# Kernel optimization log

Hardware: AMD Instinct MI355X
Metric: run time of the kernel (lower is better)

The kernel has to match this reference:

```python
import jax, jax.numpy as jnp
import numpy as np

H = 16        # num_heads
D = 128       # head_dim = hidden_size // num_heads
HID = 2048    # hidden_size
BLOCK = 64    # moba_chunk_size
TOPK = 8      # moba_topk


def setup_inputs() -> dict:
    key = jax.random.key(0)
    ks = jax.random.split(key, 5)
    B, S = 1, 2048
    hidden_states = jax.random.normal(ks[0], (B, S, HID), dtype=jnp.float32)
    scale = HID ** -0.5
    Wq = jax.random.normal(ks[1], (HID, H * D), dtype=jnp.float32) * scale
    Wk = jax.random.normal(ks[2], (HID, H * D), dtype=jnp.float32) * scale
    Wv = jax.random.normal(ks[3], (HID, H * D), dtype=jnp.float32) * scale
    Wo = jax.random.normal(ks[4], (H * D, HID), dtype=jnp.float32) * scale
    return {"hidden_states": hidden_states, "Wq": Wq, "Wk": Wk, "Wv": Wv, "Wo": Wo}


def _moba_forward(hidden_states, Wq, Wk, Wv, Wo):
    B, S, _ = hidden_states.shape
    nb = S // BLOCK
    INF = jnp.float32(jnp.inf)

    q = (hidden_states @ Wq).reshape(B, S, H, D)
    k = (hidden_states @ Wk).reshape(B, S, H, D)
    v = (hidden_states @ Wv).reshape(B, S, H, D)

    # MoBA gating: mean-pooled key per block -> [B, nb, H, D]
    kg = k.reshape(B, nb, BLOCK, H, D).mean(axis=2)
    gate = jnp.einsum('bshd,bnhd->bhsn', q, kg)  # [B,H,S,nb]

    pos = jnp.arange(S)
    qb = pos // BLOCK                 # query's own block
    blk = jnp.arange(nb)
    is_self = qb[:, None] == blk[None, :]                      # self block always selected
    not_past = pos[:, None] < (blk[None, :] + 1) * BLOCK       # blocks not fully in the past
    gate = jnp.where(is_self, INF, jnp.where(not_past, -INF, gate))

    kk = min(TOPK, nb)
    topv, topi = jax.lax.top_k(gate, kk)                       # [B,H,S,kk]
    thresh = topv.min(axis=-1, keepdims=True)
    idx_mask = (topi[..., None] == blk).any(axis=-2)           # [B,H,S,nb]
    need = (gate >= thresh) & idx_mask
    gate_bias = jnp.where(need, 0.0, -INF)                     # additive block mask

    sm_scale = D ** -0.5
    qk = jnp.einsum('bshd,bthd->bhst', q, k) * sm_scale        # [B,H,S,S]
    qk = qk.reshape(B, H, S, nb, BLOCK) + gate_bias[..., None]
    qk = qk.reshape(B, H, S, S)
    causal = pos[:, None] >= pos[None, :]
    qk = jnp.where(causal, qk, -INF)

    p = jax.nn.softmax(qk, axis=-1)
    o = jnp.einsum('bhst,bthd->bshd', p, v).reshape(B, S, H * D)
    return o @ Wo


def reference(hidden_states, Wq, Wk, Wv, Wo):
    # Returns (output, attentions=None, past_key_values=None) in the original;
    # only the output tensor matters for correctness.
    return _moba_forward(hidden_states, Wq, Wk, Wv, Wo)
```

## Files before the change

kernel.cpp:

```cpp
#include <hip/hip_runtime.h>
#include <hip/hip_bf16.h>
#include <stdint.h>
#include <stddef.h>


using bh = __bf16;
typedef __bf16 bhx8 __attribute__((ext_vector_type(8)));
typedef __bf16 bhx4 __attribute__((ext_vector_type(4)));
typedef float  f32x4 __attribute__((ext_vector_type(4)));

#define SEQ   2048
#define HIDN  2048
#define NHEAD 16
#define HDIM  128
#define NBLK  32
#define BLKSZ 64
#define NQKV  6144
#define NGATE 512
#define LDK   72
#define LDC   136
#define PSTRIDE ((size_t)SEQ * NGATE)

#define GLDS16(gsrc, ldst)                                                     \
  __builtin_amdgcn_global_load_lds(                                            \
      (const __attribute__((address_space(1))) uint32_t*)(gsrc),               \
      (__attribute__((address_space(3))) uint32_t*)(ldst), 16, 0, 0)

__global__ __launch_bounds__(256) void split_f32(const float* __restrict__ in,
                                                 bh* __restrict__ hi, bh* __restrict__ lo, int n) {
  int i = (blockIdx.x * 256 + threadIdx.x) * 4;
  if (i >= n) return;
  float4 v = *(const float4*)(in + i);
  bhx4 h4, l4;
  float vv[4] = {v.x, v.y, v.z, v.w};
#pragma unroll
  for (int e = 0; e < 4; e++) {
    bh h = (bh)vv[e];
    h4[e] = h;
    l4[e] = (bh)(vv[e] - (float)h);
  }
  *(bhx4*)(hi + i) = h4;
  *(bhx4*)(lo + i) = l4;
}

__global__ __launch_bounds__(256) void transpose_cast(const float* __restrict__ in,
                                                      bh* __restrict__ out, int R, int C) {
  __shared__ float tile[32][33];
  int tx = threadIdx.x, ty = threadIdx.y;
  int c0 = blockIdx.x * 32, r0 = blockIdx.y * 32;
#pragma unroll
  for (int i = 0; i < 4; i++)
    tile[ty + i * 8][tx] = in[(size_t)(r0 + ty + i * 8) * C + c0 + tx];
  __syncthreads();
#pragma unroll
  for (int i = 0; i < 4; i++)
    out[(size_t)(c0 + ty + i * 8) * R + r0 + tx] = (bh)tile[tx][ty + i * 8];
}

__global__ __launch_bounds__(256) void gemm_bt(const bh* __restrict__ A, const bh* __restrict__ BT,
                                               bh* __restrict__ Cb, int M, int N, int K) {
  __shared__ __align__(16) bh smem[2 * 128 * LDK];
  bh* As = smem;
  bh* Bs = smem + 128 * LDK;
  const int t = threadIdx.x;
  const int L = t & 63, w = t >> 6;
  const int wm = w & 1, wn = w >> 1;
  const int quad = L >> 4, lo = L & 15;
  const int m0 = blockIdx.y * 128, n0 = blockIdx.x * 128;

  f32x4 acc[4][4];
#pragma unroll
  for (int i = 0; i < 4; i++)
#pragma unroll
    for (int j = 0; j < 4; j++) acc[i][j] = (f32x4){0.f, 0.f, 0.f, 0.f};

  for (int k0 = 0; k0 < K; k0 += 64) {
#pragma unroll
    for (int c = 0; c < 4; c++) {
      int i = c * 256 + t;
      int row = i >> 3, cg = i & 7;
      *(uint4*)&As[row * LDK + cg * 8] = *(const uint4*)(A + (size_t)(m0 + row) * K + k0 + cg * 8);
      *(uint4*)&Bs[row * LDK + cg * 8] = *(const uint4*)(BT + (size_t)(n0 + row) * K + k0 + cg * 8);
    }
    __syncthreads();
#pragma unroll
    for (int ks = 0; ks < 2; ks++) {
      bhx8 af[4], bf_[4];
#pragma unroll
      for (int i = 0; i < 4; i++)
        af[i] = *(const bhx8*)&As[(wm * 64 + i * 16 + lo) * LDK + ks * 32 + quad * 8];
#pragma unroll
      for (int j = 0; j < 4; j++)
        bf_[j] = *(const bhx8*)&Bs[(wn * 64 + j * 16 + lo) * LDK + ks * 32 + quad * 8];
#pragma unroll
      for (int i = 0; i < 4; i++)
#pragma unroll
        for (int j = 0; j < 4; j++)
          acc[i][j] = __builtin_amdgcn_mfma_f32_16x16x32_bf16(af[i], bf_[j], acc[i][j], 0, 0, 0);
    }
    __syncthreads();
  }

  bh* Cs = smem;
#pragma unroll
  for (int i = 0; i < 4; i++)
#pragma unroll
    for (int j = 0; j < 4; j++)
#pragma unroll
      for (int r = 0; r < 4; r++)
        Cs[(wm * 64 + i * 16 + quad * 4 + r) * LDC + wn * 64 + j * 16 + lo] = (bh)acc[i][j][r];
  __syncthreads();
#pragma unroll
  for (int it = 0; it < 8; it++) {
    int idx = it * 256 + t;
    int row = idx >> 4, cg = idx & 15;
    *(uint4*)(Cb + (size_t)(m0 + row) * N + n0 + cg * 8) = *(const uint4*)&Cs[row * LDC + cg * 8];
  }
}

__global__ __launch_bounds__(256) void gemm_bt128f(const bh* __restrict__ A, const bh* __restrict__ BT,
                                                   float* __restrict__ Cf, int M, int N, int K) {
  __shared__ __align__(16) bh smem[2 * 128 * LDK];
  bh* As = smem;
  bh* Bs = smem + 128 * LDK;
  const int t = threadIdx.x;
  const int L = t & 63, w = t >> 6;
  const int wm = w & 1, wn = w >> 1;
  const int quad = L >> 4, lo = L & 15;
  const int m0 = blockIdx.y * 128, n0 = blockIdx.x * 128;

  f32x4 acc[4][4];
#pragma unroll
  for (int i = 0; i < 4; i++)
#pragma unroll
    for (int j = 0; j < 4; j++) acc[i][j] = (f32x4){0.f, 0.f, 0.f, 0.f};

  for (int k0 = 0; k0 < K; k0 += 64) {
#pragma unroll
    for (int c = 0; c < 4; c++) {
      int i = c * 256 + t;
      int row = i >> 3, cg = i & 7;
      *(uint4*)&As[row * LDK + cg * 8] = *(const uint4*)(A + (size_t)(m0 + row) * K + k0 + cg * 8);
      *(uint4*)&Bs[row * LDK + cg * 8] = *(const uint4*)(BT + (size_t)(n0 + row) * K + k0 + cg * 8);
    }
    __syncthreads();
#pragma unroll
    for (int ks = 0; ks < 2; ks++) {
      bhx8 af[4], bf_[4];
#pragma unroll
      for (int i = 0; i < 4; i++)
        af[i] = *(const bhx8*)&As[(wm * 64 + i * 16 + lo) * LDK + ks * 32 + quad * 8];
#pragma unroll
      for (int j = 0; j < 4; j++)
        bf_[j] = *(const bhx8*)&Bs[(wn * 64 + j * 16 + lo) * LDK + ks * 32 + quad * 8];
#pragma unroll
      for (int i = 0; i < 4; i++)
#pragma unroll
        for (int j = 0; j < 4; j++)
          acc[i][j] = __builtin_amdgcn_mfma_f32_16x16x32_bf16(af[i], bf_[j], acc[i][j], 0, 0, 0);
    }
    __syncthreads();
  }

#pragma unroll
  for (int i = 0; i < 4; i++)
#pragma unroll
    for (int j = 0; j < 4; j++)
#pragma unroll
      for (int r = 0; r < 4; r++) {
        int row = m0 + wm * 64 + i * 16 + quad * 4 + r;
        int col = n0 + wn * 64 + j * 16 + lo;
        Cf[(size_t)row * N + col] = acc[i][j][r];
      }
}

__global__ __launch_bounds__(256) void gemm_gate_split(const bh* __restrict__ hs_hi,
                                                       const bh* __restrict__ hs_lo,
                                                       const bh* __restrict__ wg_hi,
                                                       const bh* __restrict__ wg_lo,
                                                       float* __restrict__ part) {
  __shared__ __align__(16) bh smem[2 * 128 * LDK];
  bh* As = smem;
  bh* Bs = smem + 128 * LDK;
  const int t = threadIdx.x;
  const int L = t & 63, w = t >> 6;
  const int wm = w & 1, wn = w >> 1;
  const int quad = L >> 4, lo = L & 15;
  const int m0 = blockIdx.y * 128, n0 = blockIdx.x * 128;
  const int z = blockIdx.z;
  const bh* Ap = ((z >> 1) == 1) ? hs_lo : hs_hi;
  const bh* Bp = ((z >> 1) == 2) ? wg_lo : wg_hi;
  const int kb = (z & 1) * 1024;

  f32x4 acc[4][4];
#pragma unroll
  for (int i = 0; i < 4; i++)
#pragma unroll
    for (int j = 0; j < 4; j++) acc[i][j] = (f32x4){0.f, 0.f, 0.f, 0.f};

  for (int k0 = 0; k0 < 1024; k0 += 64) {
#pragma unroll
    for (int c = 0; c < 4; c++) {
      int i = c * 256 + t;
      int row = i >> 3, cg = i & 7;
      *(uint4*)&As[row * LDK + cg * 8] = *(const uint4*)(Ap + (size_t)(m0 + row) * HIDN + kb + k0 + cg * 8);
      *(uint4*)&Bs[row * LDK + cg * 8] = *(const uint4*)(Bp + (size_t)(n0 + row) * HIDN + kb + k0 + cg * 8);
    }
    __syncthreads();
#pragma unroll
    for (int ks = 0; ks < 2; ks++) {
      bhx8 af[4], bf_[4];
#pragma unroll
      for (int i = 0; i < 4; i++)
        af[i] = *(const bhx8*)&As[(wm * 64 + i * 16 + lo) * LDK + ks * 32 + quad * 8];
#pragma unroll
      for (int j = 0; j < 4; j++)
        bf_[j] = *(const bhx8*)&Bs[(wn * 64 + j * 16 + lo) * LDK + ks * 32 + quad * 8];
#pragma unroll
      for (int i = 0; i < 4; i++)
#pragma unroll
        for (int j = 0; j < 4; j++)
          acc[i][j] = __builtin_amdgcn_mfma_f32_16x16x32_bf16(af[i], bf_[j], acc[i][j], 0, 0, 0);
    }
    __syncthreads();
  }

#pragma unroll
  for (int i = 0; i < 4; i++)
#pragma unroll
    for (int j = 0; j < 4; j++)
#pragma unroll
      for (int r = 0; r < 4; r++) {
        int row = m0 + wm * 64 + i * 16 + quad * 4 + r;
        int col = n0 + wn * 64 + j * 16 + lo;
        part[(size_t)z * PSTRIDE + (size_t)row * NGATE + col] = acc[i][j][r];
      }
}

__global__ __launch_bounds__(256) void hsmean_k(const float* __restrict__ hs, float* __restrict__ hsm) {
  int idx = blockIdx.x * 256 + threadIdx.x;
  int n = idx >> 11, c = idx & 2047;
  const float* p = hs + (size_t)(n * BLKSZ) * HIDN + c;
  float s = 0.f;
#pragma unroll 8
  for (int r = 0; r < BLKSZ; r++) s += p[(size_t)r * HIDN];
  hsm[idx] = s * (1.0f / 64.0f);
}

__global__ __launch_bounds__(256) void kg_partial(const float* __restrict__ hsm,
                                                  const float* __restrict__ Wk,
                                                  float* __restrict__ part) {
  __shared__ float hl[32][256];
  int c = blockIdx.x * 256 + threadIdx.x;
  int k0 = blockIdx.y * 256;
#pragma unroll 4
  for (int i = 0; i < 32; i++) hl[i][threadIdx.x] = hsm[(size_t)i * HIDN + k0 + threadIdx.x];
  __syncthreads();
  float acc[32];
#pragma unroll
  for (int n = 0; n < 32; n++) acc[n] = 0.f;
  for (int k4 = 0; k4 < 64; k4++) {
    float w0 = Wk[(size_t)(k0 + k4 * 4 + 0) * HIDN + c];
    float w1 = Wk[(size_t)(k0 + k4 * 4 + 1) * HIDN + c];
    float w2 = Wk[(size_t)(k0 + k4 * 4 + 2) * HIDN + c];
    float w3 = Wk[(size_t)(k0 + k4 * 4 + 3) * HIDN + c];
#pragma unroll
    for (int n = 0; n < 32; n++) {
      float4 hv = *(const float4*)&hl[n][k4 * 4];
      acc[n] += hv.x * w0 + hv.y * w1 + hv.z * w2 + hv.w * w3;
    }
  }
#pragma unroll
  for (int n = 0; n < 32; n++)
    part[((size_t)blockIdx.y * 32 + n) * HIDN + c] = acc[n];
}

__global__ __launch_bounds__(256) void kg_reduce8(const float* __restrict__ part, float* __restrict__ kg) {
  int idx = blockIdx.x * 256 + threadIdx.x;
  float s = 0.f;
#pragma unroll
  for (int kc = 0; kc < 8; kc++) s += part[(size_t)kc * 65536 + idx];
  kg[idx] = s;
}

__global__ __launch_bounds__(256) void wg_k(const float* __restrict__ Wq, const float* __restrict__ kg,
                                            float* __restrict__ wg) {
  __shared__ float kl[32][128];
  int h = blockIdx.y;
  int r = blockIdx.x * 256 + threadIdx.x;
  for (int i = threadIdx.x; i < 32 * 128; i += 256)
    kl[i >> 7][i & 127] = kg[(size_t)(i >> 7) * HIDN + h * HDIM + (i & 127)];
  __syncthreads();
  float acc[32];
#pragma unroll
  for (int n = 0; n < 32; n++) acc[n] = 0.f;
  const float4* wrow = (const float4*)(Wq + (size_t)r * HIDN + h * HDIM);
  for (int d4 = 0; d4 < 32; d4++) {
    float4 w = wrow[d4];
#pragma unroll
    for (int n = 0; n < 32; n++) {
      float4 kv = *(const float4*)&kl[n][d4 * 4];
      acc[n] += w.x * kv.x + w.y * kv.y + w.z * kv.z + w.w * kv.w;
    }
  }
#pragma unroll
  for (int n = 0; n < 32; n++)
    wg[(size_t)(h * 32 + n) * HIDN + r] = acc[n];
}

__global__ __launch_bounds__(256) void gate_topk(const float* __restrict__ part,
                                                 unsigned* __restrict__ bsel) {
  int w = threadIdx.x >> 6, L = threadIdx.x & 63;
  int p = blockIdx.x * 4 + w;
  int h = p >> 11, s = p & 2047;
  int qb = s >> 6;
  int n = L;
  float g = -1e30f;
  if (n == qb) g = 1e30f;
  else if (n < qb) {
    size_t off = (size_t)s * NGATE + h * 32 + n;
    g = part[off] + part[off + PSTRIDE] + part[off + 2 * PSTRIDE] +
        part[off + 3 * PSTRIDE] + part[off + 4 * PSTRIDE] + part[off + 5 * PSTRIDE];
  }
  int rank = 0;
#pragma unroll
  for (int j = 0; j < 32; j++) {
    float gj = __shfl(g, j, 64);
    if (gj > g || (gj == g && j < n)) rank++;
  }
  bool sel = (n <= qb) && (n < 32) && (rank < 8);
  unsigned long long bm = __ballot(sel);
  if (L == 0) bsel[p] = (unsigned)(bm & 0xffffffffull);
}

__global__ __launch_bounds__(256) void vtrans(const bh* __restrict__ qkv, bh* __restrict__ vt) {
  __shared__ float tile[32][33];
  int tx = threadIdx.x, ty = threadIdx.y;
  int s0 = blockIdx.x * 32, d0 = blockIdx.y * 32, h = blockIdx.z;
#pragma unroll
  for (int i = 0; i < 4; i++)
    tile[ty + i * 8][tx] = (float)qkv[(size_t)(s0 + ty + i * 8) * NQKV + 2 * HIDN + h * HDIM + d0 + tx];
  __syncthreads();
#pragma unroll
  for (int i = 0; i < 4; i++)
    vt[((size_t)h * HDIM + d0 + ty + i * 8) * SEQ + s0 + tx] = (bh)tile[tx][ty + i * 8];
}

__global__ __launch_bounds__(256) void attn(const bh* __restrict__ qkv, const bh* __restrict__ vt,
                                            const unsigned* __restrict__ bsel, bh* __restrict__ obuf) {
  __shared__ __align__(16) bh Ksm[2][64 * 128];
  __shared__ __align__(16) bh Vsm[2][128 * 64];
  __shared__ __align__(16) bh PLb[4][16 * 72];
  __shared__ unsigned ublk;
  const int t = threadIdx.x;
  const int w = t >> 6, L = t & 63;
  const int quad = L >> 4, lo = L & 15;
  const int bid = blockIdx.x;
  const int jj = bid >> 3;
  const int h = ((bid & 7) << 1) | (jj & 1);
  const int qb = (jj < 32) ? (31 - (jj >> 1)) : ((jj - 32) >> 1);
  const int s0 = qb * 64 + w * 16;

  unsigned bs[4];
#pragma unroll
  for (int r = 0; r < 4; r++) bs[r] = bsel[h * SEQ + s0 + quad * 4 + r];
  unsigned uni = bs[0] | bs[1] | bs[2] | bs[3];
  uni |= (unsigned)__shfl_xor((int)uni, 16);
  uni |= (unsigned)__shfl_xor((int)uni, 32);
  const unsigned uniw = uni;
  if (t == 0) ublk = 0;
  __syncthreads();
  if (L == 0) atomicOr(&ublk, uni);
  __syncthreads();
  const unsigned un = ublk;

  bhx8 aq[4];
  const bh* qrow = qkv + (size_t)(s0 + lo) * NQKV + h * HDIM;
#pragma unroll
  for (int ks = 0; ks < 4; ks++) aq[ks] = *(const bhx8*)(qrow + ks * 32 + quad * 8);

  f32x4 oacc[8];
#pragma unroll
  for (int j = 0; j < 8; j++) oacc[j] = (f32x4){0.f, 0.f, 0.f, 0.f};
  f32x4 lacc = (f32x4){0.f, 0.f, 0.f, 0.f};
  float mi[4] = {-1e30f, -1e30f, -1e30f, -1e30f};

  bhx8 ones8;
#pragma unroll
  for (int e = 0; e < 8; e++) ones8[e] = (bh)1.0f;

  const float scale = 0.08838834764831845f;

  auto stageKV = [&](int b, int n) {
    const char* ksrc = (const char*)(qkv + (size_t)(n * BLKSZ) * NQKV + HIDN + h * HDIM);
    const char* vsrc = (const char*)(vt + ((size_t)h * HDIM) * SEQ + n * BLKSZ);
    char* kb = (char*)&Ksm[b][0];
    char* vb = (char*)&Vsm[b][0];
#pragma unroll
    for (int it = 0; it < 4; it++) {
      int idx = it * 256 + t;
      int row = idx >> 4, x = (idx & 15) << 4;
      GLDS16(ksrc + (size_t)row * (NQKV * 2) + (x ^ ((row & 7) << 4)),
             kb + ((idx >> 6) << 10));
    }
#pragma unroll
    for (int it = 0; it < 4; it++) {
      int idx = it * 256 + t;
      int row = idx >> 3, x = (idx & 7) << 4;
      GLDS16(vsrc + (size_t)row * (SEQ * 2) + (x ^ ((row & 7) << 4)),
             vb + ((idx >> 6) << 10));
    }
  };

  unsigned rem = un;
  int ncur = (int)__builtin_ctz(rem);
  rem &= rem - 1;
  stageKV(0, ncur);
  int cur = 0;

  while (true) {
    int nnext = -1;
    if (rem) { nnext = (int)__builtin_ctz(rem); rem &= rem - 1; }
    if (nnext >= 0) {
      stageKV(cur ^ 1, nnext);
      asm volatile("s_waitcnt vmcnt(8)" ::: "memory");
    } else {
      asm volatile("s_waitcnt vmcnt(0)" ::: "memory");
    }
    __builtin_amdgcn_s_barrier();

    if ((uniw >> ncur) & 1) {
      const char* Kc = (const char*)&Ksm[cur][0];
      const char* Vc = (const char*)&Vsm[cur][0];
      const bool self = (ncur == qb);

      f32x4 sc[4];
      __builtin_amdgcn_s_setprio(1);
#pragma unroll
      for (int nt = 0; nt < 4; nt++) {
        f32x4 s4 = (f32x4){0.f, 0.f, 0.f, 0.f};
#pragma unroll
        for (int ks = 0; ks < 4; ks++) {
          const int row = nt * 16 + lo;
          bhx8 bk = *(const bhx8*)(Kc + row * 256 + ((ks * 64 + quad * 16) ^ ((row & 7) << 4)));
          s4 = __builtin_amdgcn_mfma_f32_16x16x32_bf16(aq[ks], bk, s4, 0, 0, 0);
        }
        sc[nt] = s4;
      }
      __builtin_amdgcn_s_setprio(0);

      if (self) {
#pragma unroll
        for (int nt = 0; nt < 4; nt++)
#pragma unroll
          for (int r = 0; r < 4; r++) {
            float v = sc[nt][r] * scale;
            int kpos = ncur * BLKSZ + nt * 16 + lo;
            int qpos = s0 + quad * 4 + r;
            bool ok = ((bs[r] >> ncur) & 1) && (kpos <= qpos);
            sc[nt][r] = ok ? v : -1e30f;
          }
      } else {
        float bias[4];
#pragma unroll
        for (int r = 0; r < 4; r++)
          bias[r] = ((bs[r] >> ncur) & 1) ? 0.f : -1e30f;
#pragma unroll
        for (int nt = 0; nt < 4; nt++)
#pragma unroll
          for (int r = 0; r < 4; r++)
            sc[nt][r] = sc[nt][r] * scale + bias[r];
      }
      float rm[4];
#pragma unroll
      for (int r = 0; r < 4; r++)
        rm[r] = fmaxf(fmaxf(sc[0][r], sc[1][r]), fmaxf(sc[2][r], sc[3][r]));
#pragma unroll
      for (int off = 1; off < 16; off <<= 1)
#pragma unroll
        for (int r = 0; r < 4; r++) rm[r] = fmaxf(rm[r], __shfl_xor(rm[r], off));

      bool exceed = (rm[0] > mi[0] + 8.f) || (rm[1] > mi[1] + 8.f) ||
                    (rm[2] > mi[2] + 8.f) || (rm[3] > mi[3] + 8.f);
      if (__any(exceed)) {
        float alpha[4];
#pragma unroll
        for (int r = 0; r < 4; r++) {
          float nm = fmaxf(mi[r], rm[r]);
          alpha[r] = __expf(mi[r] - nm);
          mi[r] = nm;
        }
#pragma unroll
        for (int j = 0; j < 8; j++)
#pragma unroll
          for (int r = 0; r < 4; r++) oacc[j][r] *= alpha[r];
#pragma unroll
        for (int r = 0; r < 4; r++) lacc[r] *= alpha[r];
      }

#pragma unroll
      for (int nt = 0; nt < 4; nt++)
#pragma unroll
        for (int r = 0; r < 4; r++) {
          float sv = sc[nt][r];
          float pv = (sv > -1e29f) ? __expf(sv - mi[r]) : 0.f;
          PLb[w][(quad * 4 + r) * 72 + nt * 16 + lo] = (bh)pv;
        }

      __builtin_amdgcn_s_setprio(1);
#pragma unroll
      for (int kk = 0; kk < 2; kk++) {
        bhx8 pa = *(const bhx8*)&PLb[w][lo * 72 + kk * 32 + quad * 8];
        lacc = __builtin_amdgcn_mfma_f32_16x16x32_bf16(pa, ones8, lacc, 0, 0, 0);
#pragma unroll
        for (int j = 0; j < 8; j++) {
          const int row = j * 16 + lo;
          bhx8 vv = *(const bhx8*)(Vc + row * 128 + ((kk * 64 + quad * 16) ^ ((row & 7) << 4)));
          oacc[j] = __builtin_amdgcn_mfma_f32_16x16x32_bf16(pa, vv, oacc[j], 0, 0, 0);
        }
      }
      __builtin_amdgcn_s_setprio(0);
    }

    __builtin_amdgcn_s_barrier();
    if (nnext < 0) break;
    ncur = nnext;
    cur ^= 1;
  }

#pragma unroll
  for (int j = 0; j < 8; j++)
#pragma unroll
    for (int r = 0; r < 4; r++) {
      int row = s0 + quad * 4 + r;
      int col = h * HDIM + j * 16 + lo;
      obuf[(size_t)row * HIDN + col] = (bh)(oacc[j][r] / lacc[r]);
    }
}

extern "C" void kernel_launch(void* const* d_in, const int* in_sizes, int n_in,
                              void* d_out, int out_size, void* d_ws, size_t ws_size,
                              hipStream_t stream) {
  const float* hs = (const float*)d_in[0];
  const float* Wq = (const float*)d_in[1];
  const float* Wk = (const float*)d_in[2];
  const float* Wv = (const float*)d_in[3];
  const float* Wo = (const float*)d_in[4];

  char* ws = (char*)d_ws;
  bh* hs_hi = (bh*)ws;            ws += (size_t)SEQ * HIDN * 2;
  bh* hs_lo = (bh*)ws;            ws += (size_t)SEQ * HIDN * 2;
  bh* wqkvT = (bh*)ws;            ws += (size_t)NQKV * HIDN * 2;
  bh* woT = (bh*)ws;              ws += (size_t)HIDN * HIDN * 2;
  bh* qkv = (bh*)ws;              ws += (size_t)SEQ * NQKV * 2;
  bh* vt = (bh*)ws;               ws += (size_t)NHEAD * HDIM * SEQ * 2;
  bh* obuf = (bh*)ws;             ws += (size_t)SEQ * HIDN * 2;
  float* hsm = (float*)ws;        ws += (size_t)NBLK * HIDN * 4;
  float* kg_part = (float*)ws;    ws += (size_t)8 * NBLK * HIDN * 4;
  float* kg = (float*)ws;         ws += (size_t)NBLK * HIDN * 4;
  float* wg = (float*)ws;         ws += (size_t)NGATE * HIDN * 4;
  bh* wg_hi = (bh*)ws;            ws += (size_t)NGATE * HIDN * 2;
  bh* wg_lo = (bh*)ws;            ws += (size_t)NGATE * HIDN * 2;
  unsigned* bsel = (unsigned*)ws; ws += (size_t)NHEAD * SEQ * 4;
  float* gpart = (float*)wqkvT;

  split_f32<<<(SEQ * HIDN) / 1024, 256, 0, stream>>>(hs, hs_hi, hs_lo, SEQ * HIDN);
  transpose_cast<<<dim3(64, 64), dim3(32, 8), 0, stream>>>(Wq, wqkvT, HIDN, HIDN);
  transpose_cast<<<dim3(64, 64), dim3(32, 8), 0, stream>>>(Wk, wqkvT + (size_t)HIDN * HIDN, HIDN, HIDN);
  transpose_cast<<<dim3(64, 64), dim3(32, 8), 0, stream>>>(Wv, wqkvT + (size_t)2 * HIDN * HIDN, HIDN, HIDN);
  transpose_cast<<<dim3(64, 64), dim3(32, 8), 0, stream>>>(Wo, woT, HIDN, HIDN);

  gemm_bt<<<dim3(NQKV / 128, SEQ / 128), 256, 0, stream>>>(hs_hi, wqkvT, qkv, SEQ, NQKV, HIDN);

  hsmean_k<<<(NBLK * HIDN) / 256, 256, 0, stream>>>(hs, hsm);
  kg_partial<<<dim3(8, 8), 256, 0, stream>>>(hsm, Wk, kg_part);
  kg_reduce8<<<(NBLK * HIDN) / 256, 256, 0, stream>>>(kg_part, kg);
  wg_k<<<dim3(8, NHEAD), 256, 0, stream>>>(Wq, kg, wg);
  split_f32<<<(NGATE * HIDN) / 1024, 256, 0, stream>>>(wg, wg_hi, wg_lo, NGATE * HIDN);
  gemm_gate_split<<<dim3(NGATE / 128, SEQ / 128, 6), 256, 0, stream>>>(hs_hi, hs_lo, wg_hi, wg_lo, gpart);
  gate_topk<<<(NHEAD * SEQ) / 4, 256, 0, stream>>>(gpart, bsel);

  vtrans<<<dim3(SEQ / 32, HDIM / 32, NHEAD), dim3(32, 8), 0, stream>>>(qkv, vt);
  attn<<<dim3(NBLK * NHEAD), 256, 0, stream>>>(qkv, vt, bsel, obuf);

  gemm_bt128f<<<dim3(HIDN / 128, SEQ / 128), 256, 0, stream>>>(obuf, woT, (float*)d_out, SEQ, HIDN, HIDN);
}
```

Before: 489.0 us.

## Stage GEMM tiles via direct global-to-LDS loads with XOR swizzle; merge transposes

The three bf16 GEMM kernels now copy A/B tiles straight from global memory into LDS with global_load_lds, replacing the register round-trip. The padded LDS layout is swapped for an unpadded 128-byte row layout with an XOR swizzle so the MFMA fragment reads avoid bank conflicts. The four weight transpose-cast launches are merged into one launch using blockIdx.z. The swizzle on the source offset together with the fixed per-wave LDS destination must match the reader's XOR pattern, so a mismatch would give wrong results.

```diff
diff --git a/kernel.cpp b/kernel.cpp
--- a/kernel.cpp
+++ b/kernel.cpp
@@ -17,7 +17,6 @@
 #define BLKSZ 64
 #define NQKV  6144
 #define NGATE 512
-#define LDK   72
 #define LDC   136
 #define PSTRIDE ((size_t)SEQ * NGATE)
 
@@ -43,30 +42,49 @@
   *(bhx4*)(lo + i) = l4;
 }
 
-__global__ __launch_bounds__(256) void transpose_cast(const float* __restrict__ in,
-                                                      bh* __restrict__ out, int R, int C) {
+__global__ __launch_bounds__(256) void transpose_cast4(const float* __restrict__ Wq,
+                                                       const float* __restrict__ Wk,
+                                                       const float* __restrict__ Wv,
+                                                       const float* __restrict__ Wo,
+                                                       bh* __restrict__ wqkvT, bh* __restrict__ woT) {
   __shared__ float tile[32][33];
+  const int z = blockIdx.z;
+  const float* in = (z == 0) ? Wq : (z == 1) ? Wk : (z == 2) ? Wv : Wo;
+  bh* out = (z < 3) ? (wqkvT + (size_t)z * HIDN * HIDN) : woT;
   int tx = threadIdx.x, ty = threadIdx.y;
   int c0 = blockIdx.x * 32, r0 = blockIdx.y * 32;
 #pragma unroll
   for (int i = 0; i < 4; i++)
-    tile[ty + i * 8][tx] = in[(size_t)(r0 + ty + i * 8) * C + c0 + tx];
+    tile[ty + i * 8][tx] = in[(size_t)(r0 + ty + i * 8) * HIDN + c0 + tx];
   __syncthreads();
 #pragma unroll
   for (int i = 0; i < 4; i++)
-    out[(size_t)(c0 + ty + i * 8) * R + r0 + tx] = (bh)tile[tx][ty + i * 8];
-}
+    out[(size_t)(c0 + ty + i * 8) * HIDN + r0 + tx] = (bh)tile[tx][ty + i * 8];
+}
+
+#define GEMM_STAGE_TILE(SRC, r0_, ldsbase)                                       \
+  {                                                                              \
+    _Pragma("unroll")                                                            \
+    for (int it_ = 0; it_ < 4; it_++) {                                          \
+      int idx_ = it_ * 256 + t;                                                  \
+      int row_ = idx_ >> 3, x_ = (idx_ & 7) << 4;                                \
+      GLDS16((const char*)(SRC) + (size_t)(r0_ + row_) * strideB + kbyte +       \
+                 (x_ ^ ((row_ & 7) << 4)),                                       \
+             (char*)(ldsbase) + ((idx_ >> 6) << 10));                            \
+    }                                                                            \
+  }
 
 __global__ __launch_bounds__(256) void gemm_bt(const bh* __restrict__ A, const bh* __restrict__ BT,
                                                bh* __restrict__ Cb, int M, int N, int K) {
-  __shared__ __align__(16) bh smem[2 * 128 * LDK];
+  __shared__ __align__(16) bh smem[128 * LDC];
   bh* As = smem;
-  bh* Bs = smem + 128 * LDK;
+  bh* Bs = smem + 128 * 64;
   const int t = threadIdx.x;
   const int L = t & 63, w = t >> 6;
   const int wm = w & 1, wn = w >> 1;
   const int quad = L >> 4, lo = L & 15;
   const int m0 = blockIdx.y * 128, n0 = blockIdx.x * 128;
+  const size_t strideB = (size_t)K * 2;
 
   f32x4 acc[4][4];
 #pragma unroll
@@ -75,23 +93,25 @@
     for (int j = 0; j < 4; j++) acc[i][j] = (f32x4){0.f, 0.f, 0.f, 0.f};
 
   for (int k0 = 0; k0 < K; k0 += 64) {
-#pragma unroll
-    for (int c = 0; c < 4; c++) {
-      int i = c * 256 + t;
-      int row = i >> 3, cg = i & 7;
-      *(uint4*)&As[row * LDK + cg * 8] = *(const uint4*)(A + (size_t)(m0 + row) * K + k0 + cg * 8);
-      *(uint4*)&Bs[row * LDK + cg * 8] = *(const uint4*)(BT + (size_t)(n0 + row) * K + k0 + cg * 8);
-    }
+    const size_t kbyte = (size_t)k0 * 2;
+    GEMM_STAGE_TILE(A, m0, As);
+    GEMM_STAGE_TILE(BT, n0, Bs);
     __syncthreads();
 #pragma unroll
     for (int ks = 0; ks < 2; ks++) {
       bhx8 af[4], bf_[4];
 #pragma unroll
-      for (int i = 0; i < 4; i++)
-        af[i] = *(const bhx8*)&As[(wm * 64 + i * 16 + lo) * LDK + ks * 32 + quad * 8];
-#pragma unroll
-      for (int j = 0; j < 4; j++)
-        bf_[j] = *(const bhx8*)&Bs[(wn * 64 + j * 16 + lo) * LDK + ks * 32 + quad * 8];
+      for (int i = 0; i < 4; i++) {
+        const int row = wm * 64 + i * 16 + lo;
+        af[i] = *(const bhx8*)((const char*)As + row * 128 +
+                               ((ks * 64 + quad * 16) ^ ((row & 7) << 4)));
+      }
+#pragma unroll
+      for (int j = 0; j < 4; j++) {
+        const int row = wn * 64 + j * 16 + lo;
+        bf_[j] = *(const bhx8*)((const char*)Bs + row * 128 +
+                                ((ks * 64 + quad * 16) ^ ((row & 7) << 4)));
+      }
 #pragma unroll
       for (int i = 0; i < 4; i++)
 #pragma unroll
@@ -120,14 +140,15 @@
 
 __global__ __launch_bounds__(256) void gemm_bt128f(const bh* __restrict__ A, const bh* __restrict__ BT,
                                                    float* __restrict__ Cf, int M, int N, int K) {
-  __shared__ __align__(16) bh smem[2 * 128 * LDK];
+  __shared__ __align__(16) bh smem[2 * 128 * 64];
   bh* As = smem;
-  bh* Bs = smem + 128 * LDK;
+  bh* Bs = smem + 128 * 64;
   const int t = threadIdx.x;
   const int L = t & 63, w = t >> 6;
   const int wm = w & 1, wn = w >> 1;
   const int quad = L >> 4, lo = L & 15;
   const int m0 = blockIdx.y * 128, n0 = blockIdx.x * 128;
+  const size_t strideB = (size_t)K * 2;
 
   f32x4 acc[4][4];
 #pragma unroll
@@ -136,23 +157,25 @@
     for (int j = 0; j < 4; j++) acc[i][j] = (f32x4){0.f, 0.f, 0.f, 0.f};
 
   for (int k0 = 0; k0 < K; k0 += 64) {
-#pragma unroll
-    for (int c = 0; c < 4; c++) {
-      int i = c * 256 + t;
-      int row = i >> 3, cg = i & 7;
-      *(uint4*)&As[row * LDK + cg * 8] = *(const uint4*)(A + (size_t)(m0 + row) * K + k0 + cg * 8);
-      *(uint4*)&Bs[row * LDK + cg * 8] = *(const uint4*)(BT + (size_t)(n0 + row) * K + k0 + cg * 8);
-    }
+    const size_t kbyte = (size_t)k0 * 2;
+    GEMM_STAGE_TILE(A, m0, As);
+    GEMM_STAGE_TILE(BT, n0, Bs);
     __syncthreads();
 #pragma unroll
     for (int ks = 0; ks < 2; ks++) {
       bhx8 af[4], bf_[4];
 #pragma unroll
-      for (int i = 0; i < 4; i++)
-        af[i] = *(const bhx8*)&As[(wm * 64 + i * 16 + lo) * LDK + ks * 32 + quad * 8];
-#pragma unroll
-      for (int j = 0; j < 4; j++)
-        bf_[j] = *(const bhx8*)&Bs[(wn * 64 + j * 16 + lo) * LDK + ks * 32 + quad * 8];
+      for (int i = 0; i < 4; i++) {
+        const int row = wm * 64 + i * 16 + lo;
+        af[i] = *(const bhx8*)((const char*)As + row * 128 +
+                               ((ks * 64 + quad * 16) ^ ((row & 7) << 4)));
+      }
+#pragma unroll
+      for (int j = 0; j < 4; j++) {
+        const int row = wn * 64 + j * 16 + lo;
+        bf_[j] = *(const bhx8*)((const char*)Bs + row * 128 +
+                                ((ks * 64 + quad * 16) ^ ((row & 7) << 4)));
+      }
 #pragma unroll
       for (int i = 0; i < 4; i++)
 #pragma unroll
@@ -179,9 +202,9 @@
                                                        const bh* __restrict__ wg_hi,
                                                        const bh* __restrict__ wg_lo,
                                                        float* __restrict__ part) {
-  __shared__ __align__(16) bh smem[2 * 128 * LDK];
+  __shared__ __align__(16) bh smem[2 * 128 * 64];
   bh* As = smem;
-  bh* Bs = smem + 128 * LDK;
+  bh* Bs = smem + 128 * 64;
   const int t = threadIdx.x;
   const int L = t & 63, w = t >> 6;
   const int wm = w & 1, wn = w >> 1;
@@ -191,6 +214,7 @@
   const bh* Ap = ((z >> 1) == 1) ? hs_lo : hs_hi;
   const bh* Bp = ((z >> 1) == 2) ? wg_lo : wg_hi;
   const int kb = (z & 1) * 1024;
+  const size_t strideB = (size_t)HIDN * 2;
 
   f32x4 acc[4][4];
 #pragma unroll
@@ -199,23 +223,25 @@
     for (int j = 0; j < 4; j++) acc[i][j] = (f32x4){0.f, 0.f, 0.f, 0.f};
 
   for (int k0 = 0; k0 < 1024; k0 += 64) {
-#pragma unroll
-    for (int c = 0; c < 4; c++) {
-      int i = c * 256 + t;
-      int row = i >> 3, cg = i & 7;
-      *(uint4*)&As[row * LDK + cg * 8] = *(const uint4*)(Ap + (size_t)(m0 + row) * HIDN + kb + k0 + cg * 8);
-      *(uint4*)&Bs[row * LDK + cg * 8] = *(const uint4*)(Bp + (size_t)(n0 + row) * HIDN + kb + k0 + cg * 8);
-    }
+    const size_t kbyte = (size_t)(kb + k0) * 2;
+    GEMM_STAGE_TILE(Ap, m0, As);
+    GEMM_STAGE_TILE(Bp, n0, Bs);
     __syncthreads();
 #pragma unroll
     for (int ks = 0; ks < 2; ks++) {
       bhx8 af[4], bf_[4];
 #pragma unroll
-      for (int i = 0; i < 4; i++)
-        af[i] = *(const bhx8*)&As[(wm * 64 + i * 16 + lo) * LDK + ks * 32 + quad * 8];
-#pragma unroll
-      for (int j = 0; j < 4; j++)
-        bf_[j] = *(const bhx8*)&Bs[(wn * 64 + j * 16 + lo) * LDK + ks * 32 + quad * 8];
+      for (int i = 0; i < 4; i++) {
+        const int row = wm * 64 + i * 16 + lo;
+        af[i] = *(const bhx8*)((const char*)As + row * 128 +
+                               ((ks * 64 + quad * 16) ^ ((row & 7) << 4)));
+      }
+#pragma unroll
+      for (int j = 0; j < 4; j++) {
+        const int row = wn * 64 + j * 16 + lo;
+        bf_[j] = *(const bhx8*)((const char*)Bs + row * 128 +
+                                ((ks * 64 + quad * 16) ^ ((row & 7) << 4)));
+      }
 #pragma unroll
       for (int i = 0; i < 4; i++)
 #pragma unroll
@@ -565,10 +591,7 @@
   float* gpart = (float*)wqkvT;
 
   split_f32<<<(SEQ * HIDN) / 1024, 256, 0, stream>>>(hs, hs_hi, hs_lo, SEQ * HIDN);
-  transpose_cast<<<dim3(64, 64), dim3(32, 8), 0, stream>>>(Wq, wqkvT, HIDN, HIDN);
-  transpose_cast<<<dim3(64, 64), dim3(32, 8), 0, stream>>>(Wk, wqkvT + (size_t)HIDN * HIDN, HIDN, HIDN);
-  transpose_cast<<<dim3(64, 64), dim3(32, 8), 0, stream>>>(Wv, wqkvT + (size_t)2 * HIDN * HIDN, HIDN, HIDN);
-  transpose_cast<<<dim3(64, 64), dim3(32, 8), 0, stream>>>(Wo, woT, HIDN, HIDN);
+  transpose_cast4<<<dim3(64, 64, 4), dim3(32, 8), 0, stream>>>(Wq, Wk, Wv, Wo, wqkvT, woT);
 
   gemm_bt<<<dim3(NQKV / 128, SEQ / 128), 256, 0, stream>>>(hs_hi, wqkvT, qkv, SEQ, NQKV, HIDN);
 
```

New measurement: 469.3 us. -4.0%, faster.
